# Optimization experiments

Measured on AMD Instinct MI355X. Metric: run time of the kernel, lower is better.

Reference implementation:

```python
import jax, jax.numpy as jnp
import numpy as np

T, B, IN_DIM, HIDDEN = 512, 64, 512, 1024


def setup_inputs() -> dict:
    key = jax.random.key(0)
    k1, k2, k3, k4, k5 = jax.random.split(key, 5)
    x = jax.random.normal(k1, (T, B, IN_DIM), dtype=jnp.float32)
    h0 = jax.random.normal(k2, (B, HIDDEN), dtype=jnp.float32)
    # parameters initialized like torch.rand (uniform [0,1))
    Wx = jax.random.uniform(k3, (IN_DIM, HIDDEN), dtype=jnp.float32)
    Wh = jax.random.uniform(k4, (HIDDEN, HIDDEN), dtype=jnp.float32)
    b = jax.random.uniform(k5, (1, HIDDEN), dtype=jnp.float32)
    return {"x": x, "h0": h0, "Wx": Wx, "Wh": Wh, "b": b}


def reference(x, h0, Wx, Wh, b):
    # Precompute input projections for all timesteps in one big GEMM:
    # [T, B, in_dim] @ [in_dim, hidden] -> [T, B, hidden]
    xw = jnp.einsum('tbi,ih->tbh', x, Wx) + b  # bias fused here

    def step(h, xw_t):
        h = jnp.tanh(xw_t + h @ Wh)
        return h, h

    h_last, outs = jax.lax.scan(step, h0, xw)
    return outs, h_last
```

## Files before the change

kernel.cpp:

```cpp
#include <hip/hip_runtime.h>
#include <hip/hip_bf16.h>


#define T_ 512
#define B_ 64
#define IN_ 512
#define H_ 1024
constexpr int TBH = T_ * B_ * H_;
constexpr int HB  = B_ * H_;
constexpr int GP8 = 1024 * 8;

typedef unsigned short u16;
typedef unsigned int u32;
typedef unsigned long long u64;
typedef __attribute__((ext_vector_type(8))) short short8;
typedef __attribute__((ext_vector_type(4))) float f32x4;

__device__ __forceinline__ void splitbf(float x, u16& hi, u16& lo) {
    unsigned u = __float_as_uint(x);
    hi = (u16)(u >> 16);
    float r = x - __uint_as_float(u & 0xffff0000u);
    lo = (u16)(__float_as_uint(r) >> 16);
}

__global__ void k_split4(const float4* __restrict__ in, u16* __restrict__ hi,
                         u16* __restrict__ lo, int n4) {
    int i = blockIdx.x * blockDim.x + threadIdx.x;
    int stride = gridDim.x * blockDim.x;
    for (; i < n4; i += stride) {
        float4 v = in[i];
        u16 h0,h1,h2,h3,l0,l1,l2,l3;
        splitbf(v.x,h0,l0); splitbf(v.y,h1,l1); splitbf(v.z,h2,l2); splitbf(v.w,h3,l3);
        uint2 hv, lv;
        hv.x = (unsigned)h0 | ((unsigned)h1 << 16);
        hv.y = (unsigned)h2 | ((unsigned)h3 << 16);
        lv.x = (unsigned)l0 | ((unsigned)l1 << 16);
        lv.y = (unsigned)l2 | ((unsigned)l3 << 16);
        *(uint2*)&hi[4*i] = hv;
        *(uint2*)&lo[4*i] = lv;
    }
}

__global__ void k_tsplit(const float* __restrict__ src, u16* __restrict__ hi,
                         u16* __restrict__ lo, int K, int N) {
    int id = blockIdx.x * 256 + threadIdx.x;
    if (id >= K * N) return;
    int k = id / N, n = id % N;
    u16 h, l; splitbf(src[id], h, l);
    hi[n*K + k] = h; lo[n*K + k] = l;
}

__global__ void k_h0(const float* __restrict__ h0, u32* __restrict__ hbufP) {
    int id = blockIdx.x * 256 + threadIdx.x;
    if (id >= HB) return;
    int b = id >> 10, k = id & 1023;
    u32 u = __float_as_uint(h0[id]);
    hbufP[(size_t)((b>>3)*2 + 1)*GP8 + k*8 + (b & 7)] = (u & 0xFFFFFF80u) | 127u;
}

__launch_bounds__(256, 2)
__global__ void k_gemm_xw(const u16* __restrict__ xhi, const u16* __restrict__ xlo,
                          const u16* __restrict__ wthi, const u16* __restrict__ wtlo,
                          const float* __restrict__ bias, float* __restrict__ out) {
    int bid = blockIdx.x;
    int mi = bid >> 3, ni = bid & 7;
    int m0 = mi * 128, n0 = ni * 128;
    int wave = threadIdx.x >> 6, lane = threadIdx.x & 63;
    int wr = wave >> 1, wc = wave & 1;
    int lrow = lane & 15, lk8 = (lane >> 4) * 8;
    const int rowb = m0 + wr*64 + lrow;
    const int colb = n0 + wc*64 + lrow;
    f32x4 acc[4][4] = {};
    for (int kt = 0; kt < 16; ++kt) {
        int kb = kt*32 + lk8;
        short8 ah[4], al[4], bh[4], bl[4];
#pragma unroll
        for (int mt = 0; mt < 4; ++mt) {
            ah[mt] = *(const short8*)&xhi[(size_t)(rowb + mt*16)*IN_ + kb];
            al[mt] = *(const short8*)&xlo[(size_t)(rowb + mt*16)*IN_ + kb];
        }
#pragma unroll
        for (int nt = 0; nt < 4; ++nt) {
            bh[nt] = *(const short8*)&wthi[(size_t)(colb + nt*16)*IN_ + kb];
            bl[nt] = *(const short8*)&wtlo[(size_t)(colb + nt*16)*IN_ + kb];
        }
#pragma unroll
        for (int mt = 0; mt < 4; ++mt)
#pragma unroll
            for (int nt = 0; nt < 4; ++nt) {
                acc[mt][nt] = __builtin_amdgcn_mfma_f32_16x16x32_bf16(ah[mt], bh[nt], acc[mt][nt], 0,0,0);
                acc[mt][nt] = __builtin_amdgcn_mfma_f32_16x16x32_bf16(ah[mt], bl[nt], acc[mt][nt], 0,0,0);
                acc[mt][nt] = __builtin_amdgcn_mfma_f32_16x16x32_bf16(al[mt], bh[nt], acc[mt][nt], 0,0,0);
            }
    }
    int orow0 = m0 + wr*64 + 4*(lane >> 4);
#pragma unroll
    for (int nt = 0; nt < 4; ++nt) {
        int col = n0 + wc*64 + nt*16 + (lane & 15);
        float bv = bias[col];
#pragma unroll
        for (int mt = 0; mt < 4; ++mt)
#pragma unroll
            for (int r = 0; r < 4; ++r)
                out[(size_t)(orow0 + mt*16 + r)*H_ + col] = acc[mt][nt][r] + bv;
    }
}

__global__ void k_gemm_f32(const float* __restrict__ A, const float* __restrict__ Bw,
                           const float* __restrict__ bias, float* __restrict__ out) {
    __shared__ float As[32][65];
    __shared__ float Bs[32][65];
    int n0 = blockIdx.x * 64, m0 = blockIdx.y * 64;
    int tid = threadIdx.x;
    int tr = tid >> 4, tc = tid & 15;
    float acc[4][4] = {};
    for (int kc = 0; kc < IN_; kc += 32) {
#pragma unroll
        for (int it = 0; it < 8; ++it) {
            int id = tid + 256*it;
            int k = id & 31, m = id >> 5;
            As[k][m] = A[(size_t)(m0 + m)*IN_ + kc + k];
        }
#pragma unroll
        for (int it = 0; it < 8; ++it) {
            int id = tid + 256*it;
            int n = id & 63, kk = id >> 6;
            Bs[kk][n] = Bw[(size_t)(kc + kk)*H_ + n0 + n];
        }
        __syncthreads();
#pragma unroll
        for (int kk = 0; kk < 32; ++kk) {
            float a[4], b[4];
#pragma unroll
            for (int i = 0; i < 4; ++i) a[i] = As[kk][tr*4+i];
#pragma unroll
            for (int j = 0; j < 4; ++j) b[j] = Bs[kk][tc*4+j];
#pragma unroll
            for (int i = 0; i < 4; ++i)
#pragma unroll
                for (int j = 0; j < 4; ++j) acc[i][j] += a[i]*b[j];
        }
        __syncthreads();
    }
#pragma unroll
    for (int i = 0; i < 4; ++i)
#pragma unroll
        for (int j = 0; j < 4; ++j)
            out[(size_t)(m0 + tr*4 + i)*H_ + n0 + tc*4 + j] = acc[i][j] + bias[n0 + tc*4 + j];
}

__launch_bounds__(512, 1)
__global__ void k_scan(const float* __restrict__ wh,
                       float* __restrict__ out,
                       u32* __restrict__ hbufP) {
    int bid = blockIdx.x;
    int g = bid >> 4, cw = bid & 15;
    int row_g = g * 8;
    int wave = threadIdx.x >> 6, lane = threadIdx.x & 63;
    int ks = wave & 3, ch = wave >> 2;
    int n0 = cw*64 + ch*32;
    int lrow = lane & 15, lk8 = (lane >> 4) * 8;
    __shared__ float partial[8 * 8 * 33];
    __shared__ float hx[8 * 1030];

    short8 bh[2][8], bl[2][8];
#pragma unroll
    for (int nt = 0; nt < 2; ++nt) {
        int col = n0 + nt*16 + lrow;
#pragma unroll
        for (int kt = 0; kt < 8; ++kt) {
            int kbase = ks*256 + kt*32 + lk8;
            short8 h8, l8;
#pragma unroll
            for (int j = 0; j < 8; ++j) {
                u16 hh, ll; splitbf(wh[(size_t)(kbase + j)*H_ + col], hh, ll);
                h8[j] = (short)hh; l8[j] = (short)ll;
            }
            bh[nt][kt] = h8; bl[nt][kt] = l8;
        }
    }

    const int ec  = threadIdx.x >> 2;
    const int er0 = (threadIdx.x & 3) * 2;
    const bool epi = (threadIdx.x < 256);
    const int ech = (ec >> 5) & 1;
    const int ecl = ec & 31;

    float xw0 = 0.f, xw1 = 0.f;
    if (epi) {
        xw0 = out[(size_t)(row_g + er0    )*H_ + cw*64 + ec];
        xw1 = out[(size_t)(row_g + er0 + 1)*H_ + cw*64 + ec];
    }

    const int bcol = wave*128 + (lane >> 2);
    const int brow = 2 * (lane & 3);

    u64 raw[8];
    u32 pend = 0xFFu;
    {
        const u64* sb = (const u64*)(hbufP + (size_t)(g*2 + 1)*GP8) + wave*512;
#pragma unroll
        for (int i = 0; i < 8; ++i)
            raw[i] = __hip_atomic_load(sb + i*64 + lane, __ATOMIC_RELAXED,
                                       __HIP_MEMORY_SCOPE_AGENT);
    }

    for (int t = 0; t < T_; ++t) {
        const u32 want = 64u | (u32)((t - 1) & 63);
        const u64 want64 = ((u64)want << 32) | (u64)want;
        const int par = t & 1;
        const u64* sb = (const u64*)(hbufP + (size_t)(g*2 + ((t+1)&1))*GP8) + wave*512;

        for (;;) {
            u32 np = 0;
#pragma unroll
            for (int i = 0; i < 8; ++i)
                if (pend & (1u << i)) {
                    u64 bad = (raw[i] ^ want64) & 0x0000007F0000007FULL;
                    if (__any(bad != 0)) np |= 1u << i;
                }
            u32 progress = pend ^ np;
            pend = np;
            if (pend == 0) break;
            if (!progress) __builtin_amdgcn_s_sleep(1);
#pragma unroll
            for (int i = 0; i < 8; ++i)
                if (pend & (1u << i))
                    raw[i] = __hip_atomic_load(sb + i*64 + lane, __ATOMIC_RELAXED,
                                               __HIP_MEMORY_SCOPE_AGENT);
        }
#pragma unroll
        for (int i = 0; i < 8; ++i) {
            int col = bcol + i*16;
            hx[brow*1030 + col]     = __uint_as_float((u32)raw[i]);
            hx[(brow+1)*1030 + col] = __uint_as_float((u32)(raw[i] >> 32));
        }
        __syncthreads();

        f32x4 acc[2][2] = {};
#pragma unroll
        for (int kt = 0; kt < 8; ++kt) {
            int p = kt & 1;
            short8 ah, al;
            int cb = (lrow & 7)*1030 + ks*256 + kt*32 + lk8;
#pragma unroll
            for (int j = 0; j < 8; ++j) {
                u32 bits = __float_as_uint(hx[cb + j]);
                ah[j] = (short)(bits >> 16);
                float r = __uint_as_float(bits & 0xFFFFFF80u)
                        - __uint_as_float(bits & 0xFFFF0000u);
                al[j] = (short)(__float_as_uint(r) >> 16);
            }
#pragma unroll
            for (int nt = 0; nt < 2; ++nt) {
                acc[nt][p] = __builtin_amdgcn_mfma_f32_16x16x32_bf16(ah, bh[nt][kt], acc[nt][p], 0,0,0);
                acc[nt][p] = __builtin_amdgcn_mfma_f32_16x16x32_bf16(ah, bl[nt][kt], acc[nt][p], 0,0,0);
                acc[nt][p] = __builtin_amdgcn_mfma_f32_16x16x32_bf16(al, bh[nt][kt], acc[nt][p], 0,0,0);
            }
        }
        if (lane < 32) {
            int r0 = 4 * (lane >> 4);
#pragma unroll
            for (int nt = 0; nt < 2; ++nt) {
                int c = nt*16 + lrow;
#pragma unroll
                for (int r = 0; r < 4; ++r)
                    partial[((ch*4 + ks)*8 + r0 + r)*33 + c] = acc[nt][0][r] + acc[nt][1][r];
            }
        }

        if (t + 1 < T_) {
            const u64* sbn = (const u64*)(hbufP + (size_t)(g*2 + par)*GP8) + wave*512;
#pragma unroll
            for (int i = 0; i < 8; ++i)
                raw[i] = __hip_atomic_load(sbn + i*64 + lane, __ATOMIC_RELAXED,
                                           __HIP_MEMORY_SCOPE_AGENT);
            pend = 0xFFu;
        }

        __syncthreads();
        if (epi) {
            float s0 = xw0, s1 = xw1;
#pragma unroll
            for (int w = 0; w < 4; ++w) {
                s0 += partial[((ech*4 + w)*8 + er0    )*33 + ecl];
                s1 += partial[((ech*4 + w)*8 + er0 + 1)*33 + ecl];
            }
            float y0 = tanhf(s0), y1 = tanhf(s1);
            const u32 tagt = 64u | (u32)(t & 63);
            u32 b0 = (__float_as_uint(y0) & 0xFFFFFF80u) | tagt;
            u32 b1 = (__float_as_uint(y1) & 0xFFFFFF80u) | tagt;
            u32* hnb = hbufP + (size_t)(g*2 + par)*GP8 + (cw*64 + ec)*8 + er0;
            (void)__hip_atomic_exchange((u64*)hnb, ((u64)b1 << 32) | (u64)b0,
                                        __ATOMIC_RELAXED, __HIP_MEMORY_SCOPE_AGENT);
            int gb0 = row_g + er0;
            out[(size_t)(t*B_ + gb0    )*H_ + cw*64 + ec] = y0;
            out[(size_t)(t*B_ + gb0 + 1)*H_ + cw*64 + ec] = y1;
            if (t == T_-1) {
                out[(size_t)TBH + (size_t)gb0*H_ + cw*64 + ec] = y0;
                out[(size_t)TBH + (size_t)(gb0+1)*H_ + cw*64 + ec] = y1;
            }
            if (t + 1 < T_) {
                xw0 = out[(size_t)((t+1)*B_ + gb0    )*H_ + cw*64 + ec];
                xw1 = out[(size_t)((t+1)*B_ + gb0 + 1)*H_ + cw*64 + ec];
            }
        }
    }
}

extern "C" void kernel_launch(void* const* d_in, const int* in_sizes, int n_in,
                              void* d_out, int out_size, void* d_ws, size_t ws_size,
                              hipStream_t stream) {
    const float* x    = (const float*)d_in[0];
    const float* h0   = (const float*)d_in[1];
    const float* Wx   = (const float*)d_in[2];
    const float* Wh   = (const float*)d_in[3];
    const float* bias = (const float*)d_in[4];
    float* out = (float*)d_out;

    const size_t nX = (size_t)T_ * B_ * IN_;
    const size_t nWx = (size_t)IN_ * H_;
    const size_t hbufB = (size_t)16 * GP8 * sizeof(u32);
    const size_t FULL_NEED = 2*nX*2 + 2*nWx*2 + hbufB;
    const size_t SAFE_NEED = hbufB;
    if (ws_size < SAFE_NEED) return;

    bool full = ws_size >= FULL_NEED;
    u16 *xhi = nullptr, *xlo = nullptr, *wthi = nullptr, *wtlo = nullptr;
    u32* hbufP;
    if (full) {
        xhi  = (u16*)d_ws;
        xlo  = xhi + nX;
        wthi = xlo + nX;
        wtlo = wthi + nWx;
        hbufP = (u32*)(wtlo + nWx);
    } else {
        hbufP = (u32*)d_ws;
    }

    hipMemsetAsync(hbufP, 0, hbufB, stream);
    k_h0<<<HB/256, 256, 0, stream>>>(h0, hbufP);
    if (full) {
        k_split4<<<2048, 256, 0, stream>>>((const float4*)x, xhi, xlo, (int)(nX/4));
        k_tsplit<<<(int)(nWx/256), 256, 0, stream>>>(Wx, wthi, wtlo, IN_, H_);
        k_gemm_xw<<<2048, 256, 0, stream>>>(xhi, xlo, wthi, wtlo, bias, out);
    } else {
        k_gemm_f32<<<dim3(16, 512), 256, 0, stream>>>(x, Wx, bias, out);
    }
    k_scan<<<128, 512, 0, stream>>>(Wh, out, hbufP);
}
```

Baseline: 2.112 ms.

## Split scan block into producer waves polling h and consumer MFMA waves

The scan block grows to 12 waves: four dedicated loader waves poll the global tagged h buffer and write it into a double-buffered LDS tile, signalling per-chunk readiness with LDS flags. Eight compute waves wait only on the chunks they need, and the epilogue waits on a completion counter instead of block-wide __syncthreads. The intent is to overlap the cross-block polling and the LDS fill with the MFMA work and to remove the two barriers per timestep. In exchange, the spin loops on LDS atomics add contention and more registers per block, and the flag and counter protocol on double buffers is delicate to get right.

Result: slower. 2.832 ms (+34.1%).

```diff
diff --git a/kernel.cpp b/kernel.cpp
--- a/kernel.cpp
+++ b/kernel.cpp
@@ -149,7 +149,7 @@
             out[(size_t)(m0 + tr*4 + i)*H_ + n0 + tc*4 + j] = acc[i][j] + bias[n0 + tc*4 + j];
 }
 
-__launch_bounds__(512, 1)
+__launch_bounds__(768, 1)
 __global__ void k_scan(const float* __restrict__ wh,
                        float* __restrict__ out,
                        u32* __restrict__ hbufP) {
@@ -157,11 +157,78 @@
     int g = bid >> 4, cw = bid & 15;
     int row_g = g * 8;
     int wave = threadIdx.x >> 6, lane = threadIdx.x & 63;
-    int ks = wave & 3, ch = wave >> 2;
-    int n0 = cw*64 + ch*32;
-    int lrow = lane & 15, lk8 = (lane >> 4) * 8;
-    __shared__ float partial[8 * 8 * 33];
-    __shared__ float hx[8 * 1030];
+    __shared__ float hx[2 * 8 * 1030];
+    __shared__ float partial[2 * 8 * 8 * 33];
+    __shared__ int flagS[2][8];
+    __shared__ int compCnt[2];
+
+    if (threadIdx.x < 16) flagS[threadIdx.x >> 3][threadIdx.x & 7] = 0;
+    if (threadIdx.x < 2)  compCnt[threadIdx.x] = 0;
+    __syncthreads();
+
+    if (wave >= 8) {
+        const int cwv = wave - 8;
+        const int bcol_off = (lane >> 2);
+        const int brow = 2 * (lane & 3);
+        for (int t = 0; t < T_; ++t) {
+            const int p = t & 1;
+            if (t >= 2) {
+                int need = 8 * (t >> 1);
+                while (__hip_atomic_load(&compCnt[p], __ATOMIC_ACQUIRE,
+                                         __HIP_MEMORY_SCOPE_WORKGROUP) < need)
+                    __builtin_amdgcn_s_sleep(2);
+            }
+            const u32 want = 64u | (u32)((t - 1) & 63);
+            const u64 want64 = ((u64)want << 32) | (u64)want;
+            const u64* sb = (const u64*)(hbufP + (size_t)(g*2 + ((t+1)&1))*GP8);
+            u64 raw[16];
+#pragma unroll
+            for (int s = 0; s < 2; ++s)
+#pragma unroll
+                for (int i = 0; i < 8; ++i)
+                    raw[s*8+i] = __hip_atomic_load(sb + (2*cwv+s)*512 + i*64 + lane,
+                                                   __ATOMIC_RELAXED, __HIP_MEMORY_SCOPE_AGENT);
+            u32 pend = 3;
+            for (;;) {
+                u32 np = 0;
+#pragma unroll
+                for (int s = 0; s < 2; ++s) {
+                    if (!(pend & (1u << s))) continue;
+                    u64 bad = 0;
+#pragma unroll
+                    for (int i = 0; i < 8; ++i)
+                        bad |= (raw[s*8+i] ^ want64) & 0x0000007F0000007FULL;
+                    if (__any(bad != 0)) { np |= 1u << s; continue; }
+                    int Kb = (2*cwv + s)*128 + bcol_off;
+                    float* hxp = hx + p*(8*1030);
+#pragma unroll
+                    for (int i = 0; i < 8; ++i) {
+                        int k = Kb + i*16;
+                        hxp[brow*1030 + k]     = __uint_as_float((u32)raw[s*8+i]);
+                        hxp[(brow+1)*1030 + k] = __uint_as_float((u32)(raw[s*8+i] >> 32));
+                    }
+                    if (lane == 0)
+                        __hip_atomic_store(&flagS[p][2*cwv+s], t + 1, __ATOMIC_RELEASE,
+                                           __HIP_MEMORY_SCOPE_WORKGROUP);
+                }
+                if (np == 0) break;
+                if (np == pend) __builtin_amdgcn_s_sleep(1);
+                pend = np;
+#pragma unroll
+                for (int s = 0; s < 2; ++s)
+                    if (pend & (1u << s))
+#pragma unroll
+                        for (int i = 0; i < 8; ++i)
+                            raw[s*8+i] = __hip_atomic_load(sb + (2*cwv+s)*512 + i*64 + lane,
+                                                           __ATOMIC_RELAXED, __HIP_MEMORY_SCOPE_AGENT);
+            }
+        }
+        return;
+    }
+
+    const int ks = wave & 3, ch = wave >> 2;
+    const int n0 = cw*64 + ch*32;
+    const int lrow = lane & 15, lk8 = (lane >> 4) * 8;
 
     short8 bh[2][8], bl[2][8];
 #pragma unroll
@@ -192,105 +259,67 @@
         xw1 = out[(size_t)(row_g + er0 + 1)*H_ + cw*64 + ec];
     }
 
-    const int bcol = wave*128 + (lane >> 2);
-    const int brow = 2 * (lane & 3);
-
-    u64 raw[8];
-    u32 pend = 0xFFu;
-    {
-        const u64* sb = (const u64*)(hbufP + (size_t)(g*2 + 1)*GP8) + wave*512;
-#pragma unroll
-        for (int i = 0; i < 8; ++i)
-            raw[i] = __hip_atomic_load(sb + i*64 + lane, __ATOMIC_RELAXED,
-                                       __HIP_MEMORY_SCOPE_AGENT);
-    }
-
     for (int t = 0; t < T_; ++t) {
-        const u32 want = 64u | (u32)((t - 1) & 63);
-        const u64 want64 = ((u64)want << 32) | (u64)want;
-        const int par = t & 1;
-        const u64* sb = (const u64*)(hbufP + (size_t)(g*2 + ((t+1)&1))*GP8) + wave*512;
-
-        for (;;) {
-            u32 np = 0;
-#pragma unroll
-            for (int i = 0; i < 8; ++i)
-                if (pend & (1u << i)) {
-                    u64 bad = (raw[i] ^ want64) & 0x0000007F0000007FULL;
-                    if (__any(bad != 0)) np |= 1u << i;
+        const int p = t & 1;
+        const float* hxp = hx + p*(8*1030);
+        f32x4 acc[2][2] = {};
+
+#pragma unroll
+        for (int half = 0; half < 2; ++half) {
+            while (__hip_atomic_load(&flagS[p][2*ks + half], __ATOMIC_ACQUIRE,
+                                     __HIP_MEMORY_SCOPE_WORKGROUP) < t + 1) {  }
+#pragma unroll
+            for (int kt = half*4; kt < half*4 + 4; ++kt) {
+                int pp = kt & 1;
+                short8 ah, al;
+                int cb = (lane & 7)*1030 + ks*256 + kt*32 + lk8;
+#pragma unroll
+                for (int j = 0; j < 8; ++j) {
+                    u32 bits = __float_as_uint(hxp[cb + j]);
+                    ah[j] = (short)(bits >> 16);
+                    float r = __uint_as_float(bits & 0xFFFFFF80u)
+                            - __uint_as_float(bits & 0xFFFF0000u);
+                    al[j] = (short)(__float_as_uint(r) >> 16);
                 }
-            u32 progress = pend ^ np;
-            pend = np;
-            if (pend == 0) break;
-            if (!progress) __builtin_amdgcn_s_sleep(1);
-#pragma unroll
-            for (int i = 0; i < 8; ++i)
-                if (pend & (1u << i))
-                    raw[i] = __hip_atomic_load(sb + i*64 + lane, __ATOMIC_RELAXED,
-                                               __HIP_MEMORY_SCOPE_AGENT);
-        }
-#pragma unroll
-        for (int i = 0; i < 8; ++i) {
-            int col = bcol + i*16;
-            hx[brow*1030 + col]     = __uint_as_float((u32)raw[i]);
-            hx[(brow+1)*1030 + col] = __uint_as_float((u32)(raw[i] >> 32));
-        }
-        __syncthreads();
-
-        f32x4 acc[2][2] = {};
-#pragma unroll
-        for (int kt = 0; kt < 8; ++kt) {
-            int p = kt & 1;
-            short8 ah, al;
-            int cb = (lrow & 7)*1030 + ks*256 + kt*32 + lk8;
-#pragma unroll
-            for (int j = 0; j < 8; ++j) {
-                u32 bits = __float_as_uint(hx[cb + j]);
-                ah[j] = (short)(bits >> 16);
-                float r = __uint_as_float(bits & 0xFFFFFF80u)
-                        - __uint_as_float(bits & 0xFFFF0000u);
-                al[j] = (short)(__float_as_uint(r) >> 16);
-            }
-#pragma unroll
-            for (int nt = 0; nt < 2; ++nt) {
-                acc[nt][p] = __builtin_amdgcn_mfma_f32_16x16x32_bf16(ah, bh[nt][kt], acc[nt][p], 0,0,0);
-                acc[nt][p] = __builtin_amdgcn_mfma_f32_16x16x32_bf16(ah, bl[nt][kt], acc[nt][p], 0,0,0);
-                acc[nt][p] = __builtin_amdgcn_mfma_f32_16x16x32_bf16(al, bh[nt][kt], acc[nt][p], 0,0,0);
+#pragma unroll
+                for (int nt = 0; nt < 2; ++nt) {
+                    acc[nt][pp] = __builtin_amdgcn_mfma_f32_16x16x32_bf16(ah, bh[nt][kt], acc[nt][pp], 0,0,0);
+                    acc[nt][pp] = __builtin_amdgcn_mfma_f32_16x16x32_bf16(ah, bl[nt][kt], acc[nt][pp], 0,0,0);
+                    acc[nt][pp] = __builtin_amdgcn_mfma_f32_16x16x32_bf16(al, bh[nt][kt], acc[nt][pp], 0,0,0);
+                }
             }
         }
         if (lane < 32) {
             int r0 = 4 * (lane >> 4);
+            float* pp = partial + p*2112 + (ch*4 + ks)*264;
 #pragma unroll
             for (int nt = 0; nt < 2; ++nt) {
                 int c = nt*16 + lrow;
 #pragma unroll
                 for (int r = 0; r < 4; ++r)
-                    partial[((ch*4 + ks)*8 + r0 + r)*33 + c] = acc[nt][0][r] + acc[nt][1][r];
-            }
-        }
-
-        if (t + 1 < T_) {
-            const u64* sbn = (const u64*)(hbufP + (size_t)(g*2 + par)*GP8) + wave*512;
-#pragma unroll
-            for (int i = 0; i < 8; ++i)
-                raw[i] = __hip_atomic_load(sbn + i*64 + lane, __ATOMIC_RELAXED,
-                                           __HIP_MEMORY_SCOPE_AGENT);
-            pend = 0xFFu;
-        }
-
-        __syncthreads();
+                    pp[(r0 + r)*33 + c] = acc[nt][0][r] + acc[nt][1][r];
+            }
+        }
+        if (lane == 0)
+            __hip_atomic_fetch_add(&compCnt[p], 1, __ATOMIC_RELEASE,
+                                   __HIP_MEMORY_SCOPE_WORKGROUP);
+
         if (epi) {
+            const int need = 8 * ((t >> 1) + 1);
+            while (__hip_atomic_load(&compCnt[p], __ATOMIC_ACQUIRE,
+                                     __HIP_MEMORY_SCOPE_WORKGROUP) < need) {  }
             float s0 = xw0, s1 = xw1;
+            const float* pb = partial + p*2112;
 #pragma unroll
             for (int w = 0; w < 4; ++w) {
-                s0 += partial[((ech*4 + w)*8 + er0    )*33 + ecl];
-                s1 += partial[((ech*4 + w)*8 + er0 + 1)*33 + ecl];
+                s0 += pb[((ech*4 + w)*8 + er0    )*33 + ecl];
+                s1 += pb[((ech*4 + w)*8 + er0 + 1)*33 + ecl];
             }
             float y0 = tanhf(s0), y1 = tanhf(s1);
             const u32 tagt = 64u | (u32)(t & 63);
             u32 b0 = (__float_as_uint(y0) & 0xFFFFFF80u) | tagt;
             u32 b1 = (__float_as_uint(y1) & 0xFFFFFF80u) | tagt;
-            u32* hnb = hbufP + (size_t)(g*2 + par)*GP8 + (cw*64 + ec)*8 + er0;
+            u32* hnb = hbufP + (size_t)(g*2 + p)*GP8 + (cw*64 + ec)*8 + er0;
             (void)__hip_atomic_exchange((u64*)hnb, ((u64)b1 << 32) | (u64)b0,
                                         __ATOMIC_RELAXED, __HIP_MEMORY_SCOPE_AGENT);
             int gb0 = row_g + er0;
@@ -347,5 +376,5 @@
     } else {
         k_gemm_f32<<<dim3(16, 512), 256, 0, stream>>>(x, Wx, bias, out);
     }
-    k_scan<<<128, 512, 0, stream>>>(Wh, out, hbufP);
-}
+    k_scan<<<128, 768, 0, stream>>>(Wh, out, hbufP);
+}
```

## Replace scan-step block barrier with per-slice LDS flags and double-buffered h

Applied to the files above, without the earlier changes.

Each wave now loads and publishes a k-slice of the hidden state into a double-buffered LDS tile and raises a workgroup-scoped flag. It computes the half of its K range it owns right away, then spins only on its partner wave's flag before doing the other half. This takes out one __syncthreads per timestep so MFMA work can start before every wave's h slice has arrived. The cost is double LDS for hx and partial, plus spin-waiting on LDS flags. The row index also changes from lrow&7 to lane&7.

Result: slower. 5.043 ms (+138.8%).

```diff
diff --git a/kernel.cpp b/kernel.cpp
--- a/kernel.cpp
+++ b/kernel.cpp
@@ -160,8 +160,15 @@
     int ks = wave & 3, ch = wave >> 2;
     int n0 = cw*64 + ch*32;
     int lrow = lane & 15, lk8 = (lane >> 4) * 8;
-    __shared__ float partial[8 * 8 * 33];
-    __shared__ float hx[8 * 1030];
+    const int slice  = 2*ks + ch;
+    const int pslice = 2*ks + 1 - ch;
+
+    __shared__ float hx[2][8 * 1030];
+    __shared__ float partial[2][8 * 8 * 33];
+    __shared__ int flagS[2][8];
+
+    if (threadIdx.x < 16) flagS[threadIdx.x >> 3][threadIdx.x & 7] = 0;
+    __syncthreads();
 
     short8 bh[2][8], bl[2][8];
 #pragma unroll
@@ -192,13 +199,13 @@
         xw1 = out[(size_t)(row_g + er0 + 1)*H_ + cw*64 + ec];
     }
 
-    const int bcol = wave*128 + (lane >> 2);
+    const int bcol = slice*128 + (lane >> 2);
     const int brow = 2 * (lane & 3);
 
     u64 raw[8];
     u32 pend = 0xFFu;
     {
-        const u64* sb = (const u64*)(hbufP + (size_t)(g*2 + 1)*GP8) + wave*512;
+        const u64* sb = (const u64*)(hbufP + (size_t)(g*2 + 1)*GP8) + slice*512;
 #pragma unroll
         for (int i = 0; i < 8; ++i)
             raw[i] = __hip_atomic_load(sb + i*64 + lane, __ATOMIC_RELAXED,
@@ -208,8 +215,8 @@
     for (int t = 0; t < T_; ++t) {
         const u32 want = 64u | (u32)((t - 1) & 63);
         const u64 want64 = ((u64)want << 32) | (u64)want;
-        const int par = t & 1;
-        const u64* sb = (const u64*)(hbufP + (size_t)(g*2 + ((t+1)&1))*GP8) + wave*512;
+        const int p = t & 1;
+        const u64* sb = (const u64*)(hbufP + (size_t)(g*2 + ((t+1)&1))*GP8) + slice*512;
 
         for (;;) {
             u32 np = 0;
@@ -229,48 +236,66 @@
                     raw[i] = __hip_atomic_load(sb + i*64 + lane, __ATOMIC_RELAXED,
                                                __HIP_MEMORY_SCOPE_AGENT);
         }
-#pragma unroll
-        for (int i = 0; i < 8; ++i) {
-            int col = bcol + i*16;
-            hx[brow*1030 + col]     = __uint_as_float((u32)raw[i]);
-            hx[(brow+1)*1030 + col] = __uint_as_float((u32)(raw[i] >> 32));
-        }
-        __syncthreads();
+        {
+            float* hxp = hx[p];
+#pragma unroll
+            for (int i = 0; i < 8; ++i) {
+                int col = bcol + i*16;
+                hxp[brow*1030 + col]     = __uint_as_float((u32)raw[i]);
+                hxp[(brow+1)*1030 + col] = __uint_as_float((u32)(raw[i] >> 32));
+            }
+        }
+        if (lane == 0)
+            __hip_atomic_store(&flagS[p][slice], t + 1, __ATOMIC_RELEASE,
+                               __HIP_MEMORY_SCOPE_WORKGROUP);
+        asm volatile("s_waitcnt lgkmcnt(0)" ::: "memory");
+        __builtin_amdgcn_sched_barrier(0);
 
         f32x4 acc[2][2] = {};
-#pragma unroll
-        for (int kt = 0; kt < 8; ++kt) {
-            int p = kt & 1;
-            short8 ah, al;
-            int cb = (lrow & 7)*1030 + ks*256 + kt*32 + lk8;
-#pragma unroll
-            for (int j = 0; j < 8; ++j) {
-                u32 bits = __float_as_uint(hx[cb + j]);
-                ah[j] = (short)(bits >> 16);
-                float r = __uint_as_float(bits & 0xFFFFFF80u)
-                        - __uint_as_float(bits & 0xFFFF0000u);
-                al[j] = (short)(__float_as_uint(r) >> 16);
-            }
-#pragma unroll
-            for (int nt = 0; nt < 2; ++nt) {
-                acc[nt][p] = __builtin_amdgcn_mfma_f32_16x16x32_bf16(ah, bh[nt][kt], acc[nt][p], 0,0,0);
-                acc[nt][p] = __builtin_amdgcn_mfma_f32_16x16x32_bf16(ah, bl[nt][kt], acc[nt][p], 0,0,0);
-                acc[nt][p] = __builtin_amdgcn_mfma_f32_16x16x32_bf16(al, bh[nt][kt], acc[nt][p], 0,0,0);
+        const float* hxp = hx[p];
+#pragma unroll
+        for (int half = 0; half < 2; ++half) {
+            const int kt0 = (half == 0) ? ch*4 : (1-ch)*4;
+            if (half == 1) {
+                while (__hip_atomic_load(&flagS[p][pslice], __ATOMIC_ACQUIRE,
+                                         __HIP_MEMORY_SCOPE_WORKGROUP) < t + 1) {  }
+            }
+#pragma unroll
+            for (int k4 = 0; k4 < 4; ++k4) {
+                const int kt = kt0 + k4;
+                const int pp = kt & 1;
+                short8 ah, al;
+                int cb = (lane & 7)*1030 + ks*256 + kt*32 + lk8;
+#pragma unroll
+                for (int j = 0; j < 8; ++j) {
+                    u32 bits = __float_as_uint(hxp[cb + j]);
+                    ah[j] = (short)(bits >> 16);
+                    float r = __uint_as_float(bits & 0xFFFFFF80u)
+                            - __uint_as_float(bits & 0xFFFF0000u);
+                    al[j] = (short)(__float_as_uint(r) >> 16);
+                }
+#pragma unroll
+                for (int nt = 0; nt < 2; ++nt) {
+                    acc[nt][pp] = __builtin_amdgcn_mfma_f32_16x16x32_bf16(ah, bh[nt][kt], acc[nt][pp], 0,0,0);
+                    acc[nt][pp] = __builtin_amdgcn_mfma_f32_16x16x32_bf16(ah, bl[nt][kt], acc[nt][pp], 0,0,0);
+                    acc[nt][pp] = __builtin_amdgcn_mfma_f32_16x16x32_bf16(al, bh[nt][kt], acc[nt][pp], 0,0,0);
+                }
             }
         }
         if (lane < 32) {
             int r0 = 4 * (lane >> 4);
+            float* pp = partial[p] + (ch*4 + ks)*264;
 #pragma unroll
             for (int nt = 0; nt < 2; ++nt) {
                 int c = nt*16 + lrow;
 #pragma unroll
                 for (int r = 0; r < 4; ++r)
-                    partial[((ch*4 + ks)*8 + r0 + r)*33 + c] = acc[nt][0][r] + acc[nt][1][r];
+                    pp[(r0 + r)*33 + c] = acc[nt][0][r] + acc[nt][1][r];
             }
         }
 
         if (t + 1 < T_) {
-            const u64* sbn = (const u64*)(hbufP + (size_t)(g*2 + par)*GP8) + wave*512;
+            const u64* sbn = (const u64*)(hbufP + (size_t)(g*2 + p)*GP8) + slice*512;
 #pragma unroll
             for (int i = 0; i < 8; ++i)
                 raw[i] = __hip_atomic_load(sbn + i*64 + lane, __ATOMIC_RELAXED,
@@ -281,16 +306,17 @@
         __syncthreads();
         if (epi) {
             float s0 = xw0, s1 = xw1;
+            const float* pb = partial[p];
 #pragma unroll
             for (int w = 0; w < 4; ++w) {
-                s0 += partial[((ech*4 + w)*8 + er0    )*33 + ecl];
-                s1 += partial[((ech*4 + w)*8 + er0 + 1)*33 + ecl];
+                s0 += pb[((ech*4 + w)*8 + er0    )*33 + ecl];
+                s1 += pb[((ech*4 + w)*8 + er0 + 1)*33 + ecl];
             }
             float y0 = tanhf(s0), y1 = tanhf(s1);
             const u32 tagt = 64u | (u32)(t & 63);
             u32 b0 = (__float_as_uint(y0) & 0xFFFFFF80u) | tagt;
             u32 b1 = (__float_as_uint(y1) & 0xFFFFFF80u) | tagt;
-            u32* hnb = hbufP + (size_t)(g*2 + par)*GP8 + (cw*64 + ec)*8 + er0;
+            u32* hnb = hbufP + (size_t)(g*2 + p)*GP8 + (cw*64 + ec)*8 + er0;
             (void)__hip_atomic_exchange((u64*)hnb, ((u64)b1 << 32) | (u64)b0,
                                         __ATOMIC_RELAXED, __HIP_MEMORY_SCOPE_AGENT);
             int gb0 = row_g + er0;
```

## Add XCD-local fast handoff path for recurrent hidden-state exchange

Applied to the files above, without the earlier changes.

Remaps scan blocks so each batch group's 16 blocks land round-robin on the same XCD, records each block's XCC_ID, and when all blocks of a group share an XCD, polls a second hidden-state buffer with sc0 loads (coherent at the shared L2) instead of device-scope atomics. Every step is written to both buffers, and the atomic buffer stays as a fallback after 64 failed fast polls. The goal is lower per-timestep inter-block synchronisation latency by keeping the handoff in the local L2 rather than going through device-coherent memory. It costs an extra atomic store per step, a startup rendezvous among blocks, and it relies on the hardware's workgroup-to-XCD placement and cache coherence semantics.

New measurement: 2.391 ms. 13.2% more time.

```diff
diff --git a/kernel.cpp b/kernel.cpp
--- a/kernel.cpp
+++ b/kernel.cpp
@@ -21,6 +21,28 @@
     hi = (u16)(u >> 16);
     float r = x - __uint_as_float(u & 0xffff0000u);
     lo = (u16)(__float_as_uint(r) >> 16);
+}
+
+__device__ __forceinline__ void fast_load8(const u64* sb_lane, u64 f[8]) {
+    u64 r0,r1,r2,r3,r4,r5,r6,r7;
+    asm volatile(
+        "global_load_dwordx2 %0, %8, off sc0\n\t"
+        "global_load_dwordx2 %1, %8, off offset:512 sc0\n\t"
+        "global_load_dwordx2 %2, %8, off offset:1024 sc0\n\t"
+        "global_load_dwordx2 %3, %8, off offset:1536 sc0\n\t"
+        "global_load_dwordx2 %4, %8, off offset:2048 sc0\n\t"
+        "global_load_dwordx2 %5, %8, off offset:2560 sc0\n\t"
+        "global_load_dwordx2 %6, %8, off offset:3072 sc0\n\t"
+        "global_load_dwordx2 %7, %8, off offset:3584 sc0\n\t"
+        "s_waitcnt vmcnt(0)"
+        : "=&v"(r0), "=&v"(r1), "=&v"(r2), "=&v"(r3),
+          "=&v"(r4), "=&v"(r5), "=&v"(r6), "=&v"(r7)
+        : "v"((u64)sb_lane) : "memory");
+    f[0]=r0; f[1]=r1; f[2]=r2; f[3]=r3; f[4]=r4; f[5]=r5; f[6]=r6; f[7]=r7;
+}
+
+__device__ __forceinline__ void fast_store(u64* p, u64 v) {
+    asm volatile("global_atomic_swap_x2 %0, %1, off" :: "v"((u64)p), "v"(v) : "memory");
 }
 
 __global__ void k_split4(const float4* __restrict__ in, u16* __restrict__ hi,
@@ -50,12 +72,16 @@
     hi[n*K + k] = h; lo[n*K + k] = l;
 }
 
-__global__ void k_h0(const float* __restrict__ h0, u32* __restrict__ hbufP) {
+__global__ void k_h0(const float* __restrict__ h0, u32* __restrict__ hbufP,
+                     u32* __restrict__ hbufF) {
     int id = blockIdx.x * 256 + threadIdx.x;
     if (id >= HB) return;
     int b = id >> 10, k = id & 1023;
     u32 u = __float_as_uint(h0[id]);
-    hbufP[(size_t)((b>>3)*2 + 1)*GP8 + k*8 + (b & 7)] = (u & 0xFFFFFF80u) | 127u;
+    u32 tv = (u & 0xFFFFFF80u) | 127u;
+    size_t off = (size_t)((b>>3)*2 + 1)*GP8 + k*8 + (b & 7);
+    hbufP[off] = tv;
+    hbufF[off] = tv;
 }
 
 __launch_bounds__(256, 2)
@@ -152,9 +178,11 @@
 __launch_bounds__(512, 1)
 __global__ void k_scan(const float* __restrict__ wh,
                        float* __restrict__ out,
-                       u32* __restrict__ hbufP) {
+                       u32* __restrict__ hbufP,
+                       u32* __restrict__ hbufF,
+                       u32* __restrict__ meta) {
     int bid = blockIdx.x;
-    int g = bid >> 4, cw = bid & 15;
+    int g = bid & 7, cw = bid >> 3;
     int row_g = g * 8;
     int wave = threadIdx.x >> 6, lane = threadIdx.x & 63;
     int ks = wave & 3, ch = wave >> 2;
@@ -162,7 +190,14 @@
     int lrow = lane & 15, lk8 = (lane >> 4) * 8;
     __shared__ float partial[8 * 8 * 33];
     __shared__ float hx[8 * 1030];
-
+    __shared__ int s_fast;
+
+    if (threadIdx.x == 0) {
+        u32 xcd;
+        asm volatile("s_getreg_b32 %0, hwreg(HW_REG_XCC_ID)" : "=s"(xcd));
+        __hip_atomic_store(&meta[bid], xcd | 0x100u, __ATOMIC_RELAXED,
+                           __HIP_MEMORY_SCOPE_AGENT);
+    }
     short8 bh[2][8], bl[2][8];
 #pragma unroll
     for (int nt = 0; nt < 2; ++nt) {
@@ -179,6 +214,21 @@
             bh[nt][kt] = h8; bl[nt][kt] = l8;
         }
     }
+    if (wave == 0) {
+        u32 v; int done;
+        do {
+            v = (lane < 16) ? __hip_atomic_load(&meta[g + 8*lane], __ATOMIC_RELAXED,
+                                                __HIP_MEMORY_SCOPE_AGENT)
+                            : 0xFFFFFFFFu;
+            done = __all(lane >= 16 || v >= 0x100u);
+            if (!done) __builtin_amdgcn_s_sleep(8);
+        } while (!done);
+        u32 v0 = __shfl(v, 0);
+        int same = __all(lane >= 16 || v == v0);
+        if (lane == 0) s_fast = same;
+    }
+    __syncthreads();
+    bool useFast = (s_fast != 0);
 
     const int ec  = threadIdx.x >> 2;
     const int er0 = (threadIdx.x & 3) * 2;
@@ -195,29 +245,50 @@
     const int bcol = wave*128 + (lane >> 2);
     const int brow = 2 * (lane & 3);
 
-    u64 raw[8];
-    u32 pend = 0xFFu;
+    u64 rawA[8];
     {
         const u64* sb = (const u64*)(hbufP + (size_t)(g*2 + 1)*GP8) + wave*512;
 #pragma unroll
         for (int i = 0; i < 8; ++i)
-            raw[i] = __hip_atomic_load(sb + i*64 + lane, __ATOMIC_RELAXED,
-                                       __HIP_MEMORY_SCOPE_AGENT);
+            rawA[i] = __hip_atomic_load(sb + i*64 + lane, __ATOMIC_RELAXED,
+                                        __HIP_MEMORY_SCOPE_AGENT);
     }
 
     for (int t = 0; t < T_; ++t) {
         const u32 want = 64u | (u32)((t - 1) & 63);
         const u64 want64 = ((u64)want << 32) | (u64)want;
         const int par = t & 1;
-        const u64* sb = (const u64*)(hbufP + (size_t)(g*2 + ((t+1)&1))*GP8) + wave*512;
-
-        for (;;) {
+        const u64* sbA = (const u64*)(hbufP + (size_t)(g*2 + ((t+1)&1))*GP8) + wave*512;
+        const u64* sbF = (const u64*)(hbufF + (size_t)(g*2 + ((t+1)&1))*GP8) + wave*512;
+
+        u64 val[8];
+        u32 pend = 0xFFu;
+
+        if (useFast) {
+            int sw = 0;
+            while (pend && sw < 64) {
+                u64 f[8];
+                fast_load8(sbF + lane, f);
+                u32 np = pend;
+#pragma unroll
+                for (int i = 0; i < 8; ++i)
+                    if (pend & (1u << i)) {
+                        u64 bad = (f[i] ^ want64) & 0x0000007F0000007FULL;
+                        if (!__any(bad != 0)) { val[i] = f[i]; np &= ~(1u << i); }
+                    }
+                if (np == pend) __builtin_amdgcn_s_sleep(1);
+                pend = np; ++sw;
+            }
+            if (pend) useFast = false;
+        }
+        while (pend) {
             u32 np = 0;
 #pragma unroll
             for (int i = 0; i < 8; ++i)
                 if (pend & (1u << i)) {
-                    u64 bad = (raw[i] ^ want64) & 0x0000007F0000007FULL;
+                    u64 bad = (rawA[i] ^ want64) & 0x0000007F0000007FULL;
                     if (__any(bad != 0)) np |= 1u << i;
+                    else val[i] = rawA[i];
                 }
             u32 progress = pend ^ np;
             pend = np;
@@ -226,21 +297,22 @@
 #pragma unroll
             for (int i = 0; i < 8; ++i)
                 if (pend & (1u << i))
-                    raw[i] = __hip_atomic_load(sb + i*64 + lane, __ATOMIC_RELAXED,
-                                               __HIP_MEMORY_SCOPE_AGENT);
-        }
+                    rawA[i] = __hip_atomic_load(sbA + i*64 + lane, __ATOMIC_RELAXED,
+                                                __HIP_MEMORY_SCOPE_AGENT);
+        }
+
 #pragma unroll
         for (int i = 0; i < 8; ++i) {
             int col = bcol + i*16;
-            hx[brow*1030 + col]     = __uint_as_float((u32)raw[i]);
-            hx[(brow+1)*1030 + col] = __uint_as_float((u32)(raw[i] >> 32));
+            hx[brow*1030 + col]     = __uint_as_float((u32)val[i]);
+            hx[(brow+1)*1030 + col] = __uint_as_float((u32)(val[i] >> 32));
         }
         __syncthreads();
 
         f32x4 acc[2][2] = {};
 #pragma unroll
         for (int kt = 0; kt < 8; ++kt) {
-            int p = kt & 1;
+            int pp = kt & 1;
             short8 ah, al;
             int cb = (lrow & 7)*1030 + ks*256 + kt*32 + lk8;
 #pragma unroll
@@ -253,9 +325,9 @@
             }
 #pragma unroll
             for (int nt = 0; nt < 2; ++nt) {
-                acc[nt][p] = __builtin_amdgcn_mfma_f32_16x16x32_bf16(ah, bh[nt][kt], acc[nt][p], 0,0,0);
-                acc[nt][p] = __builtin_amdgcn_mfma_f32_16x16x32_bf16(ah, bl[nt][kt], acc[nt][p], 0,0,0);
-                acc[nt][p] = __builtin_amdgcn_mfma_f32_16x16x32_bf16(al, bh[nt][kt], acc[nt][p], 0,0,0);
+                acc[nt][pp] = __builtin_amdgcn_mfma_f32_16x16x32_bf16(ah, bh[nt][kt], acc[nt][pp], 0,0,0);
+                acc[nt][pp] = __builtin_amdgcn_mfma_f32_16x16x32_bf16(ah, bl[nt][kt], acc[nt][pp], 0,0,0);
+                acc[nt][pp] = __builtin_amdgcn_mfma_f32_16x16x32_bf16(al, bh[nt][kt], acc[nt][pp], 0,0,0);
             }
         }
         if (lane < 32) {
@@ -273,9 +345,8 @@
             const u64* sbn = (const u64*)(hbufP + (size_t)(g*2 + par)*GP8) + wave*512;
 #pragma unroll
             for (int i = 0; i < 8; ++i)
-                raw[i] = __hip_atomic_load(sbn + i*64 + lane, __ATOMIC_RELAXED,
-                                           __HIP_MEMORY_SCOPE_AGENT);
-            pend = 0xFFu;
+                rawA[i] = __hip_atomic_load(sbn + i*64 + lane, __ATOMIC_RELAXED,
+                                            __HIP_MEMORY_SCOPE_AGENT);
         }
 
         __syncthreads();
@@ -290,8 +361,10 @@
             const u32 tagt = 64u | (u32)(t & 63);
             u32 b0 = (__float_as_uint(y0) & 0xFFFFFF80u) | tagt;
             u32 b1 = (__float_as_uint(y1) & 0xFFFFFF80u) | tagt;
-            u32* hnb = hbufP + (size_t)(g*2 + par)*GP8 + (cw*64 + ec)*8 + er0;
-            (void)__hip_atomic_exchange((u64*)hnb, ((u64)b1 << 32) | (u64)b0,
+            u64 v64 = ((u64)b1 << 32) | (u64)b0;
+            size_t hoff = (size_t)(g*2 + par)*GP8 + (cw*64 + ec)*8 + er0;
+            fast_store((u64*)&hbufF[hoff], v64);
+            (void)__hip_atomic_exchange((u64*)&hbufP[hoff], v64,
                                         __ATOMIC_RELAXED, __HIP_MEMORY_SCOPE_AGENT);
             int gb0 = row_g + er0;
             out[(size_t)(t*B_ + gb0    )*H_ + cw*64 + ec] = y0;
@@ -321,8 +394,10 @@
     const size_t nX = (size_t)T_ * B_ * IN_;
     const size_t nWx = (size_t)IN_ * H_;
     const size_t hbufB = (size_t)16 * GP8 * sizeof(u32);
-    const size_t FULL_NEED = 2*nX*2 + 2*nWx*2 + hbufB;
-    const size_t SAFE_NEED = hbufB;
+    const size_t metaB = 128 * sizeof(u32);
+    const size_t scanB = 2*hbufB + metaB;
+    const size_t FULL_NEED = 2*nX*2 + 2*nWx*2 + scanB;
+    const size_t SAFE_NEED = scanB;
     if (ws_size < SAFE_NEED) return;
 
     bool full = ws_size >= FULL_NEED;
@@ -337,9 +412,11 @@
     } else {
         hbufP = (u32*)d_ws;
     }
-
-    hipMemsetAsync(hbufP, 0, hbufB, stream);
-    k_h0<<<HB/256, 256, 0, stream>>>(h0, hbufP);
+    u32* hbufF = hbufP + 16*GP8;
+    u32* meta  = hbufF + 16*GP8;
+
+    hipMemsetAsync(hbufP, 0, scanB, stream);
+    k_h0<<<HB/256, 256, 0, stream>>>(h0, hbufP, hbufF);
     if (full) {
         k_split4<<<2048, 256, 0, stream>>>((const float4*)x, xhi, xlo, (int)(nX/4));
         k_tsplit<<<(int)(nWx/256), 256, 0, stream>>>(Wx, wthi, wtlo, IN_, H_);
@@ -347,5 +424,5 @@
     } else {
         k_gemm_f32<<<dim3(16, 512), 256, 0, stream>>>(x, Wx, bias, out);
     }
-    k_scan<<<128, 512, 0, stream>>>(Wh, out, hbufP);
-}
+    k_scan<<<128, 512, 0, stream>>>(Wh, out, hbufP, hbufF, meta);
+}
```
